# Performance work log

Hardware: AMD Instinct MI355X
Metric: run time of the kernel (lower is better)

## Reference

```python
import jax, jax.numpy as jnp
import numpy as np

NUM_ENT = 50000
NUM_REL = 500
D = 128          # embed_dim
B = 1024         # batch of queries
K = 32           # neighbors per query


def setup_inputs() -> dict:
    key = jax.random.key(0)
    ks = jax.random.split(key, 10)
    src_idx = jax.random.randint(ks[0], (B,), 0, NUM_ENT)
    rel_idx = jax.random.randint(ks[1], (B,), 0, NUM_REL)
    ts = jax.random.randint(ks[2], (B,), 0, 365)
    ngh_node = jax.random.randint(ks[3], (B, K), 0, NUM_ENT)
    ngh_eidx = jax.random.randint(ks[4], (B, K), 0, NUM_REL)
    ngh_ts = jax.random.randint(ks[5], (B, K), 0, 365)
    # learned params (symbol table holds entities then relations, + pad row)
    symbol_emb = jax.random.normal(ks[6], (NUM_ENT + NUM_REL + 1, D), dtype=jnp.float32) * 0.02
    gcn_w_w = jax.random.normal(ks[7], (D, 2 * D), dtype=jnp.float32) * (1.0 / np.sqrt(2 * D))
    gcn_w_b = jnp.zeros((D,), dtype=jnp.float32)
    proj_w = jax.random.normal(ks[8], (D, 2 * D), dtype=jnp.float32) * (1.0 / np.sqrt(2 * D))
    proj_b = jnp.zeros((D,), dtype=jnp.float32)
    # TimeEncode params: basis_freq = 1/10**linspace(0,9,D), phase = 0
    basis_freq = jnp.asarray(1.0 / 10 ** np.linspace(0, 9, D), dtype=jnp.float32)
    phase = jnp.zeros((D,), dtype=jnp.float32)
    return {
        'src_idx': src_idx, 'rel_idx': rel_idx, 'ts': ts,
        'ngh_node': ngh_node, 'ngh_eidx': ngh_eidx, 'ngh_ts': ngh_ts,
        'symbol_emb': symbol_emb, 'gcn_w_w': gcn_w_w, 'gcn_w_b': gcn_w_b,
        'proj_w': proj_w, 'proj_b': proj_b,
        'basis_freq': basis_freq, 'phase': phase,
    }


def reference(src_idx, rel_idx, ts, ngh_node, ngh_eidx, ngh_ts,
              symbol_emb, gcn_w_w, gcn_w_b, proj_w, proj_b, basis_freq, phase):
    # --- get_node_emb for each (query, neighbor) pair ---
    mask = ngh_node >= 0                               # [B,K] valid-neighbor mask (-1 = pad)
    safe_ngh = jnp.where(mask, ngh_node, 0)
    hidden_node = symbol_emb[safe_ngh]                 # [B,K,D] entity gather
    cut_time = (ngh_ts - ts[:, None]).astype(jnp.float32)  # [B,K]
    hidden_time = jnp.cos(cut_time[..., None] * basis_freq + phase)  # [B,K,D] TimeEncode
    node_emb = jnp.einsum('bkf,df->bkd',
                          jnp.concatenate([hidden_node, hidden_time], axis=-1),
                          proj_w) + proj_b             # [B,K,D] node_emb_proj
    # --- relation embeddings (offset by num_ent into symbol table) ---
    rel_emb = symbol_emb[ngh_eidx + NUM_ENT]           # [B,K,D]
    # --- neighbor_encoder: concat -> linear -> masked mean over K -> tanh ---
    concat_emb = jnp.concatenate([node_emb, rel_emb], axis=-1)  # [B,K,2D]
    out = jnp.einsum('bkf,df->bkd', concat_emb, gcn_w_w) + gcn_w_b
    cnt = jnp.maximum(mask.sum(axis=1, keepdims=True), 1).astype(out.dtype)  # [B,1]
    sub_emb = jnp.tanh(jnp.where(mask[..., None], out, 0.0).sum(axis=1) / cnt)  # [B,D]
    # --- Distmult scoring against all entities (cut_time = 0 for all) ---
    all_time = jnp.cos(phase)                          # [D] time encoding at t=0
    all_in = jnp.concatenate(
        [symbol_emb[:NUM_ENT], jnp.broadcast_to(all_time, (NUM_ENT, D))], axis=-1)
    all_emb = all_in @ proj_w.T + proj_b               # [NUM_ENT, D]
    rel_q = symbol_emb[rel_idx + NUM_ENT]              # [B,D]
    score = (sub_emb * rel_q) @ all_emb.T              # [B, NUM_ENT]
    return score
```

## Files before the change

### kernel.cpp

```cpp
#include <hip/hip_runtime.h>
#include <hip/hip_bf16.h>

#define NUM_ENT 50000
#define NUM_REL 500
#define DIM 128
#define BQ 1024
#define KN 32
#define TBL 729
#define NTILE 256
#define XPW 68

typedef _Float16 f16x8 __attribute__((ext_vector_type(8)));
typedef _Float16 f16x4 __attribute__((ext_vector_type(4)));
typedef float f32x4 __attribute__((ext_vector_type(4)));

__global__ void prep_kernel(const float* __restrict__ gcn_w_w,
                            const float* __restrict__ gcn_w_b,
                            const float* __restrict__ proj_w,
                            const float* __restrict__ proj_b,
                            const float* __restrict__ phase,
                            const float* __restrict__ basis_freq,
                            float* __restrict__ W,
                            float* __restrict__ bias,
                            float* __restrict__ Call,
                            float* __restrict__ COS) {
    int j = blockIdx.x;
    int d = threadIdx.x;
    if (j < 256) {
        float acc = 0.f;
        for (int f = 0; f < DIM; ++f)
            acc += gcn_w_w[d * 256 + f] * proj_w[f * 256 + j];
        W[j * DIM + d] = acc;
    } else if (j < 384) {
        W[j * DIM + d] = gcn_w_w[d * 256 + 128 + (j - 256)];
    } else if (j == 384) {
        float b1 = 0.f;
        for (int f = 0; f < DIM; ++f) b1 += proj_b[f] * gcn_w_w[d * 256 + f];
        bias[d] = b1 + gcn_w_b[d];
        float cc = 0.f;
        for (int g = 0; g < DIM; ++g) cc += cosf(phase[g]) * proj_w[d * 256 + 128 + g];
        Call[d] = cc + proj_b[d];
    } else {
        int row = j - 385;
        COS[row * DIM + d] = cosf((float)(row - 364) * basis_freq[d] + phase[d]);
    }
}

__global__ __launch_bounds__(256) void query_kernel(const int* __restrict__ rel_idx,
                             const int* __restrict__ ts,
                             const int* __restrict__ ngh_node,
                             const int* __restrict__ ngh_eidx,
                             const int* __restrict__ ngh_ts,
                             const float* __restrict__ symbol_emb,
                             const float* __restrict__ proj_w,
                             const float* __restrict__ W,
                             const float* __restrict__ bias,
                             const float* __restrict__ Call,
                             const float* __restrict__ COS,
                             float* __restrict__ cOut,
                             _Float16* __restrict__ uOut) {
    int b = blockIdx.x;
    int t = threadIdx.x;
    __shared__ int sE[KN], sR[KN], sT[KN];
    __shared__ float sP[3][8][DIM];
    __shared__ float sAgg[3 * DIM];
    __shared__ float sAcc[2][DIM];
    __shared__ float sQ[DIM];
    __shared__ float sU[2][DIM];
    __shared__ float sC[2];

    if (t < KN) {
        sE[t] = ngh_node[b * KN + t];
        sR[t] = ngh_eidx[b * KN + t];
        int dt = ngh_ts[b * KN + t] - ts[b] + 364;
        sT[t] = dt < 0 ? 0 : (dt > 728 ? 728 : dt);
    }
    __syncthreads();

    int c = t & 31;
    int g = t >> 5;
    f32x4 pN = {0.f,0.f,0.f,0.f}, pC = pN, pR = pN;
    #pragma unroll
    for (int i = 0; i < 4; ++i) {
        int k = i * 8 + g;
        int e = sE[k];
        bool valid = (e >= 0);
        int es = valid ? e : 0;
        f32x4 vN = *reinterpret_cast<const f32x4*>(symbol_emb + (size_t)es * DIM + c * 4);
        f32x4 vC = *reinterpret_cast<const f32x4*>(COS + sT[k] * DIM + c * 4);
        f32x4 vR = *reinterpret_cast<const f32x4*>(symbol_emb + (size_t)(NUM_ENT + sR[k]) * DIM + c * 4);
        if (valid) { pN += vN; pC += vC; pR += vR; }
    }
    *reinterpret_cast<f32x4*>(&sP[0][g][c * 4]) = pN;
    *reinterpret_cast<f32x4*>(&sP[1][g][c * 4]) = pC;
    *reinterpret_cast<f32x4*>(&sP[2][g][c * 4]) = pR;

    int cnt = 0;
    #pragma unroll
    for (int k = 0; k < KN; ++k) cnt += (sE[k] >= 0) ? 1 : 0;
    __syncthreads();

    #pragma unroll
    for (int o = t; o < 384; o += 256) {
        float s = 0.f;
        #pragma unroll
        for (int gg = 0; gg < 8; ++gg) s += sP[o >> 7][gg][o & 127];
        sAgg[o] = s;
    }
    __syncthreads();

    int d = t & 127;
    int h = t >> 7;
    int j0 = h * 64;
    float acc = 0.f;
    #pragma unroll 8
    for (int j = 0; j < 64; ++j) acc += sAgg[j0 + j] * W[(j0 + j) * DIM + d];
    #pragma unroll 8
    for (int j = 0; j < 64; ++j) acc += sAgg[128 + j0 + j] * W[(128 + j0 + j) * DIM + d];
    #pragma unroll 8
    for (int j = 0; j < 64; ++j) acc += sAgg[256 + j0 + j] * W[(256 + j0 + j) * DIM + d];
    sAcc[h][d] = acc;
    __syncthreads();

    if (h == 0) {
        float total = sAcc[0][d] + sAcc[1][d] + (float)cnt * bias[d];
        float denom = (float)(cnt > 0 ? cnt : 1);
        float sub = tanhf(total / denom);
        sQ[d] = sub * symbol_emb[(size_t)(NUM_ENT + rel_idx[b]) * DIM + d];
    }
    __syncthreads();

    float u = 0.f;
    #pragma unroll 8
    for (int dd = 0; dd < 64; ++dd) u += sQ[j0 + dd] * proj_w[(j0 + dd) * 256 + d];
    sU[h][d] = u;

    float cp = (t < 128) ? sQ[t] * Call[t] : 0.f;
    #pragma unroll
    for (int m = 1; m < 64; m <<= 1) cp += __shfl_xor(cp, m, 64);
    if (t == 0) sC[0] = cp;
    if (t == 64) sC[1] = cp;
    __syncthreads();

    if (h == 0) uOut[b * DIM + d] = (_Float16)(sU[0][d] + sU[1][d]);
    if (t == 0) cOut[b] = sC[0] + sC[1];
}

__global__ __launch_bounds__(256) void score_kernel(const _Float16* __restrict__ U,
                                                    const float* __restrict__ S,
                                                    const float* __restrict__ cArr,
                                                    float* __restrict__ out) {
    __shared__ char smem[32768];
    int wgid = blockIdx.x;
    int swz = (wgid & 7) * 98 + (wgid >> 3);
    int xtile = swz >> 2;
    int qchunk = swz & 3;
    int n0 = xtile * NTILE;

    int t = threadIdx.x;
    int lane = t & 63;
    int wave = t >> 6;
    int lr = lane & 15;
    int lg = lane >> 4;
    int lk = lg * 8;

    f16x8 a[4][4];

    {
        const float* src = S + (size_t)n0 * DIM;
        #pragma unroll 4
        for (int i = 0; i < 16; ++i) {
            int fi = i * 256 + t;
            float4 v = *reinterpret_cast<const float4*>(src + (size_t)fi * 4);
            int r = fi >> 5;
            int k8 = (fi & 31) * 8;
            f16x4 o;
            o[0] = (_Float16)v.x; o[1] = (_Float16)v.y;
            o[2] = (_Float16)v.z; o[3] = (_Float16)v.w;
            int byte = (r * 256 + k8) ^ ((r & 7) << 4);
            *reinterpret_cast<f16x4*>(smem + byte) = o;
        }
    }
    __syncthreads();
    if (wave < 2) {
        #pragma unroll
        for (int nn = 0; nn < 4; ++nn) {
            int r = wave * 64 + nn * 16 + lr;
            int rowbase = r * 256;
            int sw = (r & 7) << 4;
            #pragma unroll
            for (int kk = 0; kk < 4; ++kk) {
                int byte = (rowbase + (kk * 32 + lk) * 2) ^ sw;
                a[nn][kk] = *reinterpret_cast<const f16x8*>(smem + byte);
            }
        }
    }
    __syncthreads();

    {
        const float* src = S + (size_t)(n0 + 128) * DIM;
        #pragma unroll 4
        for (int i = 0; i < 16; ++i) {
            int fi = i * 256 + t;
            float4 v = *reinterpret_cast<const float4*>(src + (size_t)fi * 4);
            int r = fi >> 5;
            int k8 = (fi & 31) * 8;
            f16x4 o;
            o[0] = (_Float16)v.x; o[1] = (_Float16)v.y;
            o[2] = (_Float16)v.z; o[3] = (_Float16)v.w;
            int byte = (r * 256 + k8) ^ ((r & 7) << 4);
            *reinterpret_cast<f16x4*>(smem + byte) = o;
        }
    }
    __syncthreads();
    if (wave >= 2) {
        #pragma unroll
        for (int nn = 0; nn < 4; ++nn) {
            int r = (wave - 2) * 64 + nn * 16 + lr;
            int rowbase = r * 256;
            int sw = (r & 7) << 4;
            #pragma unroll
            for (int kk = 0; kk < 4; ++kk) {
                int byte = (rowbase + (kk * 32 + lk) * 2) ^ sw;
                a[nn][kk] = *reinterpret_cast<const f16x8*>(smem + byte);
            }
        }
    }
    __syncthreads();

    float* xp = reinterpret_cast<float*>(smem + wave * 8192);

    int qbase = qchunk * 256;
    for (int qg = 0; qg < 16; ++qg) {
        int q0 = qbase + qg * 16;
        f16x8 bfr[4];
        #pragma unroll
        for (int kk = 0; kk < 4; ++kk)
            bfr[kk] = *reinterpret_cast<const f16x8*>(U + (q0 + lr) * DIM + kk * 32 + lk);
        float cv = cArr[q0 + lr];

        f32x4 acc[4];
        #pragma unroll
        for (int nn = 0; nn < 4; ++nn) acc[nn] = (f32x4){0.f, 0.f, 0.f, 0.f};

        #pragma unroll
        for (int kk = 0; kk < 4; ++kk)
            #pragma unroll
            for (int nn = 0; nn < 4; ++nn)
                acc[nn] = __builtin_amdgcn_mfma_f32_16x16x32_f16(a[nn][kk], bfr[kk], acc[nn], 0, 0, 0);

        #pragma unroll
        for (int nn = 0; nn < 4; ++nn) {
            f32x4 v = acc[nn] + cv;
            *reinterpret_cast<f32x4*>(&xp[lr * XPW + nn * 16 + lg * 4]) = v;
        }

        #pragma unroll
        for (int j = 0; j < 4; ++j) {
            int row = j * 4 + (lane >> 4);
            int q = q0 + row;
            int e = n0 + wave * 64 + (lane & 15) * 4;
            if (e < NUM_ENT) {
                f32x4 v = *reinterpret_cast<const f32x4*>(&xp[row * XPW + (lane & 15) * 4]);
                *reinterpret_cast<f32x4*>(out + (size_t)q * NUM_ENT + e) = v;
            }
        }
    }
}

extern "C" void kernel_launch(void* const* d_in, const int* in_sizes, int n_in,
                              void* d_out, int out_size, void* d_ws, size_t ws_size,
                              hipStream_t stream) {
    const int*   rel_idx    = (const int*)d_in[1];
    const int*   ts         = (const int*)d_in[2];
    const int*   ngh_node   = (const int*)d_in[3];
    const int*   ngh_eidx   = (const int*)d_in[4];
    const int*   ngh_ts     = (const int*)d_in[5];
    const float* symbol_emb = (const float*)d_in[6];
    const float* gcn_w_w    = (const float*)d_in[7];
    const float* gcn_w_b    = (const float*)d_in[8];
    const float* proj_w     = (const float*)d_in[9];
    const float* proj_b     = (const float*)d_in[10];
    const float* basis_freq = (const float*)d_in[11];
    const float* phase      = (const float*)d_in[12];
    float* out = (float*)d_out;

    char* ws = (char*)d_ws;
    float*     W    = (float*)(ws + 0);
    float*     bias = (float*)(ws + 196608);
    float*     Call = (float*)(ws + 197120);
    float*     COS  = (float*)(ws + 197632);
    float*     cArr = (float*)(ws + 570880);
    _Float16*  U    = (_Float16*)(ws + 574976);

    prep_kernel<<<385 + TBL, 128, 0, stream>>>(gcn_w_w, gcn_w_b, proj_w, proj_b,
                                               phase, basis_freq, W, bias, Call, COS);
    query_kernel<<<BQ, 256, 0, stream>>>(rel_idx, ts, ngh_node, ngh_eidx, ngh_ts,
                                         symbol_emb, proj_w, W, bias, Call, COS,
                                         cArr, U);
    score_kernel<<<784, 256, 0, stream>>>(U, symbol_emb, cArr, out);
}
```

Before: 92.37 us.

## Split query kernel into gather and batched dot kernels reusing weights across queries

The per-query kernel is split into a gather kernel that writes the aggregated neighbor sums and valid counts to workspace, and a dot kernel that handles four queries per block. Each weight load from W and proj_w is now reused across four queries, which cuts global weight traffic in the small matrix-vector stage by a factor of four. The cost is an extra kernel launch and a round-trip of the aggregates through global memory, and the dot kernel launches only 256 blocks, so fewer blocks are available to fill the GPU.

```diff
diff --git a/kernel.cpp b/kernel.cpp
--- a/kernel.cpp
+++ b/kernel.cpp
@@ -9,6 +9,7 @@
 #define TBL 729
 #define NTILE 256
 #define XPW 68
+#define QB 4
 
 typedef _Float16 f16x8 __attribute__((ext_vector_type(8)));
 typedef _Float16 f16x4 __attribute__((ext_vector_type(4)));
@@ -46,28 +47,19 @@
     }
 }
 
-__global__ __launch_bounds__(256) void query_kernel(const int* __restrict__ rel_idx,
+__global__ __launch_bounds__(256) void gather_kernel(
                              const int* __restrict__ ts,
                              const int* __restrict__ ngh_node,
                              const int* __restrict__ ngh_eidx,
                              const int* __restrict__ ngh_ts,
                              const float* __restrict__ symbol_emb,
-                             const float* __restrict__ proj_w,
-                             const float* __restrict__ W,
-                             const float* __restrict__ bias,
-                             const float* __restrict__ Call,
                              const float* __restrict__ COS,
-                             float* __restrict__ cOut,
-                             _Float16* __restrict__ uOut) {
+                             float* __restrict__ Agg,
+                             int* __restrict__ cntArr) {
     int b = blockIdx.x;
     int t = threadIdx.x;
     __shared__ int sE[KN], sR[KN], sT[KN];
     __shared__ float sP[3][8][DIM];
-    __shared__ float sAgg[3 * DIM];
-    __shared__ float sAcc[2][DIM];
-    __shared__ float sQ[DIM];
-    __shared__ float sU[2][DIM];
-    __shared__ float sC[2];
 
     if (t < KN) {
         sE[t] = ngh_node[b * KN + t];
@@ -105,45 +97,109 @@
         float s = 0.f;
         #pragma unroll
         for (int gg = 0; gg < 8; ++gg) s += sP[o >> 7][gg][o & 127];
-        sAgg[o] = s;
-    }
-    __syncthreads();
-
+        Agg[(size_t)b * 384 + o] = s;
+    }
+    if (t == 0) cntArr[b] = cnt;
+}
+
+__global__ __launch_bounds__(256) void dot_kernel(
+                             const int* __restrict__ rel_idx,
+                             const float* __restrict__ symbol_emb,
+                             const float* __restrict__ proj_w,
+                             const float* __restrict__ W,
+                             const float* __restrict__ bias,
+                             const float* __restrict__ Call,
+                             const float* __restrict__ Agg,
+                             const int* __restrict__ cntArr,
+                             float* __restrict__ cOut,
+                             _Float16* __restrict__ uOut) {
+    int b0 = blockIdx.x * QB;
+    int t = threadIdx.x;
     int d = t & 127;
     int h = t >> 7;
     int j0 = h * 64;
-    float acc = 0.f;
+    __shared__ float sA[QB * 384];
+    __shared__ float sAcc[2][QB][DIM];
+    __shared__ float sQ[QB][DIM];
+    __shared__ float sU[2][QB][DIM];
+    __shared__ float sCc[2][QB];
+
+    #pragma unroll
+    for (int o = t; o < QB * 384 / 4; o += 256)
+        *reinterpret_cast<f32x4*>(&sA[o * 4]) =
+            *reinterpret_cast<const f32x4*>(Agg + (size_t)b0 * 384 + o * 4);
+    __syncthreads();
+
+    int cw0 = cntArr[b0 + 0], cw1 = cntArr[b0 + 1];
+    int cw2 = cntArr[b0 + 2], cw3 = cntArr[b0 + 3];
+
+    float a0 = 0.f, a1 = 0.f, a2 = 0.f, a3 = 0.f;
+    #pragma unroll
+    for (int arr = 0; arr < 3; ++arr) {
+        #pragma unroll 8
+        for (int j = 0; j < 64; ++j) {
+            int o = arr * 128 + j0 + j;
+            float w = W[o * DIM + d];
+            a0 += sA[o] * w;
+            a1 += sA[384 + o] * w;
+            a2 += sA[768 + o] * w;
+            a3 += sA[1152 + o] * w;
+        }
+    }
+    sAcc[h][0][d] = a0; sAcc[h][1][d] = a1;
+    sAcc[h][2][d] = a2; sAcc[h][3][d] = a3;
+    __syncthreads();
+
+    if (h == 0) {
+        float t0 = sAcc[0][0][d] + sAcc[1][0][d] + (float)cw0 * bias[d];
+        float t1 = sAcc[0][1][d] + sAcc[1][1][d] + (float)cw1 * bias[d];
+        float t2 = sAcc[0][2][d] + sAcc[1][2][d] + (float)cw2 * bias[d];
+        float t3 = sAcc[0][3][d] + sAcc[1][3][d] + (float)cw3 * bias[d];
+        float s0 = tanhf(t0 / (float)(cw0 > 0 ? cw0 : 1));
+        float s1 = tanhf(t1 / (float)(cw1 > 0 ? cw1 : 1));
+        float s2 = tanhf(t2 / (float)(cw2 > 0 ? cw2 : 1));
+        float s3 = tanhf(t3 / (float)(cw3 > 0 ? cw3 : 1));
+        sQ[0][d] = s0 * symbol_emb[(size_t)(NUM_ENT + rel_idx[b0 + 0]) * DIM + d];
+        sQ[1][d] = s1 * symbol_emb[(size_t)(NUM_ENT + rel_idx[b0 + 1]) * DIM + d];
+        sQ[2][d] = s2 * symbol_emb[(size_t)(NUM_ENT + rel_idx[b0 + 2]) * DIM + d];
+        sQ[3][d] = s3 * symbol_emb[(size_t)(NUM_ENT + rel_idx[b0 + 3]) * DIM + d];
+    }
+    __syncthreads();
+
+    float u0 = 0.f, u1 = 0.f, u2 = 0.f, u3 = 0.f;
     #pragma unroll 8
-    for (int j = 0; j < 64; ++j) acc += sAgg[j0 + j] * W[(j0 + j) * DIM + d];
-    #pragma unroll 8
-    for (int j = 0; j < 64; ++j) acc += sAgg[128 + j0 + j] * W[(128 + j0 + j) * DIM + d];
-    #pragma unroll 8
-    for (int j = 0; j < 64; ++j) acc += sAgg[256 + j0 + j] * W[(256 + j0 + j) * DIM + d];
-    sAcc[h][d] = acc;
+    for (int dd = 0; dd < 64; ++dd) {
+        float p = proj_w[(j0 + dd) * 256 + d];
+        u0 += sQ[0][j0 + dd] * p;
+        u1 += sQ[1][j0 + dd] * p;
+        u2 += sQ[2][j0 + dd] * p;
+        u3 += sQ[3][j0 + dd] * p;
+    }
+    sU[h][0][d] = u0; sU[h][1][d] = u1;
+    sU[h][2][d] = u2; sU[h][3][d] = u3;
+
+    float cp0 = (t < 128) ? sQ[0][t] * Call[t] : 0.f;
+    float cp1 = (t < 128) ? sQ[1][t] * Call[t] : 0.f;
+    float cp2 = (t < 128) ? sQ[2][t] * Call[t] : 0.f;
+    float cp3 = (t < 128) ? sQ[3][t] * Call[t] : 0.f;
+    #pragma unroll
+    for (int m = 1; m < 64; m <<= 1) {
+        cp0 += __shfl_xor(cp0, m, 64);
+        cp1 += __shfl_xor(cp1, m, 64);
+        cp2 += __shfl_xor(cp2, m, 64);
+        cp3 += __shfl_xor(cp3, m, 64);
+    }
+    if (t == 0)  { sCc[0][0] = cp0; sCc[0][1] = cp1; sCc[0][2] = cp2; sCc[0][3] = cp3; }
+    if (t == 64) { sCc[1][0] = cp0; sCc[1][1] = cp1; sCc[1][2] = cp2; sCc[1][3] = cp3; }
     __syncthreads();
 
     if (h == 0) {
-        float total = sAcc[0][d] + sAcc[1][d] + (float)cnt * bias[d];
-        float denom = (float)(cnt > 0 ? cnt : 1);
-        float sub = tanhf(total / denom);
-        sQ[d] = sub * symbol_emb[(size_t)(NUM_ENT + rel_idx[b]) * DIM + d];
-    }
-    __syncthreads();
-
-    float u = 0.f;
-    #pragma unroll 8
-    for (int dd = 0; dd < 64; ++dd) u += sQ[j0 + dd] * proj_w[(j0 + dd) * 256 + d];
-    sU[h][d] = u;
-
-    float cp = (t < 128) ? sQ[t] * Call[t] : 0.f;
-    #pragma unroll
-    for (int m = 1; m < 64; m <<= 1) cp += __shfl_xor(cp, m, 64);
-    if (t == 0) sC[0] = cp;
-    if (t == 64) sC[1] = cp;
-    __syncthreads();
-
-    if (h == 0) uOut[b * DIM + d] = (_Float16)(sU[0][d] + sU[1][d]);
-    if (t == 0) cOut[b] = sC[0] + sC[1];
+        uOut[(size_t)(b0 + 0) * DIM + d] = (_Float16)(sU[0][0][d] + sU[1][0][d]);
+        uOut[(size_t)(b0 + 1) * DIM + d] = (_Float16)(sU[0][1][d] + sU[1][1][d]);
+        uOut[(size_t)(b0 + 2) * DIM + d] = (_Float16)(sU[0][2][d] + sU[1][2][d]);
+        uOut[(size_t)(b0 + 3) * DIM + d] = (_Float16)(sU[0][3][d] + sU[1][3][d]);
+    }
+    if (t < QB) cOut[b0 + t] = sCc[0][t] + sCc[1][t];
 }
 
 __global__ __launch_bounds__(256) void score_kernel(const _Float16* __restrict__ U,
@@ -292,11 +348,14 @@
     float*     COS  = (float*)(ws + 197632);
     float*     cArr = (float*)(ws + 570880);
     _Float16*  U    = (_Float16*)(ws + 574976);
+    float*     Agg  = (float*)(ws + 837120);
+    int*       cnt  = (int*)(ws + 2409984);
 
     prep_kernel<<<385 + TBL, 128, 0, stream>>>(gcn_w_w, gcn_w_b, proj_w, proj_b,
                                                phase, basis_freq, W, bias, Call, COS);
-    query_kernel<<<BQ, 256, 0, stream>>>(rel_idx, ts, ngh_node, ngh_eidx, ngh_ts,
-                                         symbol_emb, proj_w, W, bias, Call, COS,
-                                         cArr, U);
+    gather_kernel<<<BQ, 256, 0, stream>>>(ts, ngh_node, ngh_eidx, ngh_ts,
+                                          symbol_emb, COS, Agg, cnt);
+    dot_kernel<<<BQ / QB, 256, 0, stream>>>(rel_idx, symbol_emb, proj_w, W, bias,
+                                            Call, Agg, cnt, cArr, U);
     score_kernel<<<784, 256, 0, stream>>>(U, symbol_emb, cArr, out);
 }
```

After: 96.08 us. 4.0% more time.
